# Kernel optimization log

Hardware: AMD Instinct MI355X
Metric: run time of the kernel (lower is better)

## Reference

```python
import jax, jax.numpy as jnp
import numpy as np

B, T, D_IN = 64, 512, 512      # batch, num_steps, input_size
S, HS, H = 8, 128, 8            # mem_slots, head_size, num_heads
M = HS * H                      # mem_size = 1024
KD = HS                         # key_size defaults to head_size
NG = 2 * M                      # num_gates (gate_style='unit')
N_MLP = 2                       # attention_mlp_layers (weights SHARED: [Linear]*2)
EPS = 1e-5


def _ln(x, g, b):
    mu = jnp.mean(x, axis=-1, keepdims=True)
    var = jnp.mean((x - mu) ** 2, axis=-1, keepdims=True)
    return (x - mu) * jax.lax.rsqrt(var + EPS) * g + b


def setup_inputs() -> dict:
    key = jax.random.key(0)
    ks = jax.random.split(key, 12)
    r = lambda i, shape, s=0.02: jax.random.normal(ks[i], shape, jnp.float32) * s
    return {
        "inputs": jax.random.normal(ks[0], (B, T, D_IN), jnp.float32),
        "memory": jax.random.normal(ks[1], (B, S, M), jnp.float32),
        "Wp": r(2, (D_IN, M)), "bp": jnp.zeros((M,), jnp.float32),
        "Wq": r(3, (M, KD * H)), "bq": jnp.zeros((KD * H,), jnp.float32),
        "Wk": r(4, (M, KD * H)), "bk": jnp.zeros((KD * H,), jnp.float32),
        "Wv": r(5, (M, HS * H)), "bv": jnp.zeros((HS * H,), jnp.float32),
        "Wm": r(6, (M, M)), "bm": jnp.zeros((M,), jnp.float32),
        "g1": jnp.ones((M,), jnp.float32), "be1": jnp.zeros((M,), jnp.float32),
        "g2": jnp.ones((M,), jnp.float32), "be2": jnp.zeros((M,), jnp.float32),
        "rl_w": r(7, (M,), 1.0),                       # RepeatLinear elementwise weight
        "rl_W": r(8, (M, NG)), "rl_b": jnp.zeros((NG,), jnp.float32),
        "gl_W": r(9, (S, M, NG)), "gl_b": r(10, (S, NG), 0.02),  # GroupLinearLayer
        "input_bias": jnp.float32(0.0),
        "forget_bias": jnp.float32(1.0),
    }


def reference(inputs, memory, Wp, bp, Wq, bq, Wk, bk, Wv, bv, Wm, bm,
              g1, be1, g2, be2, rl_w, rl_W, rl_b, gl_W, gl_b,
              input_bias, forget_bias):
    # forward_step with treat_input_as_matrix=True (single num_blocks=1 block)
    x = inputs @ Wp + bp                                   # [B,T,M] projected inputs
    # multihead attention: q from memory, k/v from inputs; NO 1/sqrt(d) scaling (as in source)
    q = (memory @ Wq + bq).reshape(B, S, H, KD).transpose(0, 2, 1, 3)   # [B,H,S,kd]
    k = (x @ Wk + bk).reshape(B, T, H, KD).transpose(0, 2, 1, 3)        # [B,H,T,kd]
    v = (x @ Wv + bv).reshape(B, T, H, HS).transpose(0, 2, 1, 3)        # [B,H,T,hs]
    scores = jax.nn.softmax(jnp.einsum('bhsd,bhtd->bhst', q, k), axis=-1)
    att = jnp.einsum('bhst,bhtd->bhsd', scores, v).transpose(0, 2, 1, 3).reshape(B, S, M)
    mem1 = _ln(memory + att, g1, be1)
    mlp = mem1
    for _ in range(N_MLP):  # ModuleList([Linear]*2) => same weights applied twice
        mlp = jax.nn.relu(mlp @ Wm + bm)
    next_memory = _ln(mem1 + mlp, g2, be2)
    # gates (create_gates uses ORIGINAL memory)
    gi = jnp.mean(jax.nn.relu(rl_w * x), axis=1) @ rl_W + rl_b            # [B,NG]
    gm = jnp.einsum('bsm,smg->bsg', jnp.tanh(memory), gl_W) + gl_b        # [B,S,NG]
    gates = gm + gi[:, None, :]
    ig = jax.nn.sigmoid(gates[..., :M] + input_bias)
    fg = jax.nn.sigmoid(gates[..., M:] + forget_bias)
    next_memory = ig * jnp.tanh(next_memory) + fg * memory
    return next_memory.reshape(B, S * M)
```

## Files before the change

kernel.cpp:

```cpp
#include <hip/hip_runtime.h>
#include <hip/hip_bf16.h>

#define Bq   64
#define Tt   512
#define DIN  512
#define Ss   8
#define HSs  128
#define Hh   8
#define Mm   1024
#define KDd  128
#define NGg  2048

typedef __attribute__((ext_vector_type(8))) short bf16x8;
typedef __attribute__((ext_vector_type(4))) float f32x4;

__device__ __forceinline__ ushort f2b(float f) {
    union { float f; unsigned u; } v; v.f = f;
    unsigned r = v.u + 0x7fffu + ((v.u >> 16) & 1u);
    return (ushort)(r >> 16);
}
__device__ __forceinline__ float b2f(ushort b) {
    union { unsigned u; float f; } v; v.u = ((unsigned)b) << 16;
    return v.f;
}
__device__ __forceinline__ float blo(unsigned u) {
    union { unsigned u; float f; } v; v.u = u << 16; return v.f;
}
__device__ __forceinline__ float bhi(unsigned u) {
    union { unsigned u; float f; } v; v.u = u & 0xffff0000u; return v.f;
}

#define GLOAD_LDS16(g, l) __builtin_amdgcn_global_load_lds( \
    (const __attribute__((address_space(1))) void*)(g),     \
    (__attribute__((address_space(3))) void*)(l), 16, 0, 0)

#define LGKM0 do { asm volatile("s_waitcnt lgkmcnt(0)" ::: "memory");         \
                   __builtin_amdgcn_sched_barrier(0); } while (0)

template<int OUT_BF16>
__global__ __launch_bounds__(512)
void gemm_big(const ushort* __restrict__ A, const ushort* __restrict__ Bt,
              const float* __restrict__ bias, void* __restrict__ Cout,
              int ldc, int Kdim)
{
    extern __shared__ __align__(16) char lds[];

    const int tid  = threadIdx.x;
    const int wid  = tid >> 6;
    const int lane = tid & 63;
    const int wy   = wid >> 2;
    const int wx   = wid & 3;

    const int gx   = gridDim.x;
    const int nwg  = gx * gridDim.y;
    const int orig = blockIdx.y * gx + blockIdx.x;
    const int q8   = nwg >> 3, r8 = nwg & 7;
    const int xcd  = orig & 7, idx8 = orig >> 3;
    const int swz  = (xcd < r8 ? xcd * (q8 + 1)
                               : r8 * (q8 + 1) + (xcd - r8) * q8) + idx8;
    const int row0 = (swz / gx) * 256;
    const int col0 = (swz % gx) * 256;

    const int NT = Kdim >> 6;

    const int sr = tid >> 3;
    const int sq = (tid & 7) ^ (sr & 7);
    const ushort* Asrc = A  + (size_t)(row0 + sr) * Kdim + sq * 8;
    const ushort* Bsrc = Bt + (size_t)(col0 + sr) * Kdim + sq * 8;
    const int ldsw = wid * 1024;

    auto stage = [&](int isB, int U, int h) {
        const ushort* s = (isB ? Bsrc : Asrc) + (size_t)h * 128 * Kdim
                        + (size_t)U * 64;
        char* d = lds + (isB ? 65536 : 0) + ((((U) & 1) * 2 + h) << 14) + ldsw;
        GLOAD_LDS16(s, d);
        GLOAD_LDS16(s + (size_t)64 * Kdim, d + 8192);
    };
    auto stage_tile = [&](int U) {
        stage(0, U, 0); stage(0, U, 1); stage(1, U, 0); stage(1, U, 1);
    };

    const int l15   = lane & 15;
    const int s0_16 = (((lane >> 4)) ^ (lane & 7)) << 4;
    const int s1_16 = ((4 + (lane >> 4)) ^ (lane & 7)) << 4;
    const int aoff  = wy * 8192 + l15 * 128;
    const int boff  = wx * 4096 + l15 * 128;

    f32x4 acc[4][4][2];
#pragma unroll
    for (int p = 0; p < 4; ++p)
#pragma unroll
        for (int m = 0; m < 4; ++m)
#pragma unroll
            for (int n = 0; n < 2; ++n) acc[p][m][n] = (f32x4){0.f,0.f,0.f,0.f};

#define MFMAQ(P, AH, BH)                                                      \
    {                                                                         \
        __builtin_amdgcn_s_setprio(1);                                        \
        _Pragma("unroll")                                                     \
        for (int kk = 0; kk < 2; ++kk)                                        \
            _Pragma("unroll")                                                 \
            for (int m = 0; m < 4; ++m)                                       \
                _Pragma("unroll")                                             \
                for (int n = 0; n < 2; ++n)                                   \
                    acc[P][m][n] = __builtin_amdgcn_mfma_f32_16x16x32_bf16(   \
                        AH[kk][m], BH[kk][n], acc[P][m][n], 0, 0, 0);         \
        __builtin_amdgcn_s_setprio(0);                                        \
    }

    stage_tile(0);
    stage_tile(1);
    asm volatile("s_waitcnt vmcnt(8)" ::: "memory");
    __builtin_amdgcn_s_barrier();
    asm volatile("" ::: "memory");

    for (int U = 0; U < NT; ++U) {
        const char* Ab = lds + ((U & 1) << 15);
        const char* Bb = lds + 65536 + ((U & 1) << 15);

        bf16x8 a0[2][4], a1[2][4];
        bf16x8 b0[2][2], b1[2][2];

#pragma unroll
        for (int m = 0; m < 4; ++m) {
            a0[0][m] = *(const bf16x8*)(Ab + aoff + s0_16 + m * 2048);
            a0[1][m] = *(const bf16x8*)(Ab + aoff + s1_16 + m * 2048);
        }
#pragma unroll
        for (int n = 0; n < 2; ++n) {
            b0[0][n] = *(const bf16x8*)(Bb + boff + s0_16 + n * 2048);
            b0[1][n] = *(const bf16x8*)(Bb + boff + s1_16 + n * 2048);
        }
        LGKM0;

#pragma unroll
        for (int m = 0; m < 4; ++m) {
            a1[0][m] = *(const bf16x8*)(Ab + 16384 + aoff + s0_16 + m * 2048);
            a1[1][m] = *(const bf16x8*)(Ab + 16384 + aoff + s1_16 + m * 2048);
        }
        MFMAQ(0, a0, b0);
        LGKM0;

#pragma unroll
        for (int n = 0; n < 2; ++n) {
            b1[0][n] = *(const bf16x8*)(Bb + 16384 + boff + s0_16 + n * 2048);
            b1[1][n] = *(const bf16x8*)(Bb + 16384 + boff + s1_16 + n * 2048);
        }
        MFMAQ(1, a1, b0);
        LGKM0;

        __builtin_amdgcn_s_barrier();
        asm volatile("" ::: "memory");
        if (U + 2 < NT) stage_tile(U + 2);

        MFMAQ(3, a1, b1);
        MFMAQ(2, a0, b1);

        if (U + 2 < NT) asm volatile("s_waitcnt vmcnt(8)" ::: "memory");
        else            asm volatile("s_waitcnt vmcnt(0)" ::: "memory");
        __builtin_amdgcn_s_barrier();
        asm volatile("" ::: "memory");
    }
#undef MFMAQ

#pragma unroll
    for (int p = 0; p < 4; ++p) {
        const int rb = row0 + (p & 1) * 128 + wy * 64 + (lane >> 4) * 4;
        const int cb = col0 + (p >> 1) * 128 + wx * 32 + (lane & 15);
#pragma unroll
        for (int n = 0; n < 2; ++n) {
            const float bv = bias[cb + n * 16];
#pragma unroll
            for (int m = 0; m < 4; ++m) {
#pragma unroll
                for (int r = 0; r < 4; ++r) {
                    const float v = acc[p][m][n][r] + bv;
                    const size_t off = (size_t)(rb + m * 16 + r) * ldc + cb + n * 16;
                    if (OUT_BF16) ((ushort*)Cout)[off] = f2b(v);
                    else          ((float*)Cout)[off]  = v;
                }
            }
        }
    }
}

template<int OUT_BF16, int RELU>
__global__ __launch_bounds__(256)
void gemm_sm(const ushort* __restrict__ A, const ushort* __restrict__ Bt,
             const float* __restrict__ bias, void* __restrict__ Cout,
             int ldc, int Kdim)
{
    __shared__ __align__(16) ushort As[128 * 32];
    __shared__ __align__(16) ushort Bs[128 * 32];

    const int tid  = threadIdx.x;
    const int w    = tid >> 6;
    const int lane = tid & 63;

    const int gx   = gridDim.x;
    const int nwg  = gx * gridDim.y;
    const int orig = blockIdx.y * gx + blockIdx.x;
    const int q8   = nwg >> 3, r8 = nwg & 7;
    const int xcd  = orig & 7, idx8 = orig >> 3;
    const int swz  = (xcd < r8 ? xcd * (q8 + 1)
                               : r8 * (q8 + 1) + (xcd - r8) * q8) + idx8;
    const int row0 = (swz / gx) * 128;
    const int col0 = (swz % gx) * 128;
    const int wr   = w >> 1, wc = w & 1;

    f32x4 acc[4][4];
#pragma unroll
    for (int i = 0; i < 4; ++i)
#pragma unroll
        for (int j = 0; j < 4; ++j) acc[i][j] = (f32x4){0.f, 0.f, 0.f, 0.f};

    const ushort* Ag = A  + (size_t)(row0 + (tid >> 2)) * Kdim + (tid & 3) * 8;
    const ushort* Bg = Bt + (size_t)(col0 + (tid >> 2)) * Kdim + (tid & 3) * 8;

    for (int k0 = 0; k0 < Kdim; k0 += 32) {
        __syncthreads();
#pragma unroll
        for (int is = 0; is < 2; ++is)
            GLOAD_LDS16(Ag + (size_t)is * 64 * Kdim + k0,
                        (char*)As + (is * 256 + w * 64) * 16);
#pragma unroll
        for (int is = 0; is < 2; ++is)
            GLOAD_LDS16(Bg + (size_t)is * 64 * Kdim + k0,
                        (char*)Bs + (is * 256 + w * 64) * 16);
        asm volatile("s_waitcnt vmcnt(0)" ::: "memory");
        __syncthreads();

        bf16x8 a[4], b[4];
#pragma unroll
        for (int i = 0; i < 4; ++i) {
            a[i] = *(const bf16x8*)&As[(wr * 64 + i * 16 + (lane & 15)) * 32 + (lane >> 4) * 8];
            b[i] = *(const bf16x8*)&Bs[(wc * 64 + i * 16 + (lane & 15)) * 32 + (lane >> 4) * 8];
        }
#pragma unroll
        for (int i = 0; i < 4; ++i)
#pragma unroll
            for (int j = 0; j < 4; ++j)
                acc[i][j] = __builtin_amdgcn_mfma_f32_16x16x32_bf16(a[i], b[j], acc[i][j], 0, 0, 0);
    }

    float bsv[4];
#pragma unroll
    for (int j = 0; j < 4; ++j) bsv[j] = bias[col0 + wc * 64 + j * 16 + (lane & 15)];
#pragma unroll
    for (int i = 0; i < 4; ++i) {
        const int row = row0 + wr * 64 + i * 16 + (lane >> 4) * 4;
        const int col = col0 + wc * 64 + (lane & 15);
#pragma unroll
        for (int r = 0; r < 4; ++r) {
            const size_t off = (size_t)(row + r) * ldc + col;
#pragma unroll
            for (int j = 0; j < 4; ++j) {
                float vv = acc[i][j][r] + bsv[j];
                if (RELU) vv = fmaxf(vv, 0.f);
                if (OUT_BF16) ((ushort*)Cout)[off + j * 16] = f2b(vv);
                else          ((float*)Cout)[off + j * 16]  = vv;
            }
        }
    }
}

__global__ __launch_bounds__(256)
void transpose_to_bf16(const float* __restrict__ in, ushort* __restrict__ out,
                       int R, int C)
{
    __shared__ float t[32][33];
    const int c0 = blockIdx.x * 32, r0 = blockIdx.y * 32;
    const int tx = threadIdx.x & 31, ty = threadIdx.x >> 5;
#pragma unroll
    for (int i = 0; i < 32; i += 8)
        t[ty + i][tx] = in[(size_t)(r0 + ty + i) * C + c0 + tx];
    __syncthreads();
#pragma unroll
    for (int i = 0; i < 32; i += 8)
        out[(size_t)(c0 + ty + i) * R + r0 + tx] = f2b(t[tx][ty + i]);
}

__global__ __launch_bounds__(256)
void conv_bf16(const float* __restrict__ in, ushort* __restrict__ out)
{
    const int i = blockIdx.x * 256 + threadIdx.x;
    float4 v = ((const float4*)in)[i];
    ushort4 o;
    o.x = f2b(v.x); o.y = f2b(v.y); o.z = f2b(v.z); o.w = f2b(v.w);
    ((ushort4*)out)[i] = o;
}

__global__ __launch_bounds__(256)
void fill0(float* __restrict__ o)
{
    o[blockIdx.x * 256 + threadIdx.x] = 0.f;
}

__global__ __launch_bounds__(256)
void fuse_bias(const float* __restrict__ bp,
               const float* __restrict__ Wk, const float* __restrict__ Wv,
               const float* __restrict__ bk, const float* __restrict__ bv,
               float* __restrict__ outb)
{
    __shared__ float red[4][64];
    const int col = threadIdx.x & 63;
    const int mq  = threadIdx.x >> 6;
    const int n   = blockIdx.x * 64 + col;
    const float* W = (n < Mm) ? Wk : Wv;
    const int nn   = n & (Mm - 1);
    float s = 0.f;
    for (int m = mq * 256; m < mq * 256 + 256; ++m)
        s += bp[m] * W[(size_t)m * Mm + nn];
    red[mq][col] = s;
    __syncthreads();
    if (mq == 0) {
        float t = red[0][col] + red[1][col] + red[2][col] + red[3][col];
        outb[n] = t + ((n < Mm) ? bk[nn] : bv[nn]);
    }
}

template<int BM, int BN, int BK, int TM, int TN, int SPLITK, bool TANH_A>
__global__ __launch_bounds__(256)
void gemm_f32_sk(const float* __restrict__ A, int lda, long long sA,
                 const float* __restrict__ B, int ldb, long long sB,
                 float* __restrict__ P, int Mrows, int Ncols, int Kdim)
{
    constexpr int TX = BN / TN;
    constexpr int TY = BM / TM;
    static_assert(TX * TY == 256, "256 threads");
    constexpr int KC4   = BK / 4;
    constexpr int A_PER = (BM * BK / 4) / 256;
    constexpr int B_PER = (BK * BN / 4) / 256;

    __shared__ float As[BK][BM + 4];
    __shared__ float Bs[BK][BN];

    const int tid = threadIdx.x;
    const int tx  = tid % TX;
    const int ty  = tid / TX;
    const int zz  = blockIdx.z;
    const int zb  = zz / SPLITK;
    const int ks  = zz % SPLITK;
    A += (long long)zb * sA;
    B += (long long)zb * sB;
    const int Kslice = Kdim / SPLITK;
    const int kbeg = ks * Kslice, kend = kbeg + Kslice;
    const int row0 = blockIdx.y * BM;
    const int col0 = blockIdx.x * BN;

    float acc[TM][TN];
#pragma unroll
    for (int i = 0; i < TM; ++i)
#pragma unroll
        for (int j = 0; j < TN; ++j) acc[i][j] = 0.f;

    for (int k0 = kbeg; k0 < kend; k0 += BK) {
        __syncthreads();
#pragma unroll
        for (int l = 0; l < A_PER; ++l) {
            int idx = tid + l * 256;
            int ar  = idx / KC4;
            int ac  = (idx % KC4) * 4;
            float4 va = *(const float4*)&A[(long long)(row0 + ar) * lda + k0 + ac];
            if (TANH_A) {
                va.x = tanhf(va.x); va.y = tanhf(va.y);
                va.z = tanhf(va.z); va.w = tanhf(va.w);
            }
            As[ac + 0][ar] = va.x;
            As[ac + 1][ar] = va.y;
            As[ac + 2][ar] = va.z;
            As[ac + 3][ar] = va.w;
        }
#pragma unroll
        for (int l = 0; l < B_PER; ++l) {
            int idx = tid + l * 256;
            int br  = idx / (BN / 4);
            int bc  = (idx % (BN / 4)) * 4;
            *(float4*)&Bs[br][bc] = *(const float4*)&B[(long long)(k0 + br) * ldb + col0 + bc];
        }
        __syncthreads();
#pragma unroll
        for (int k = 0; k < BK; ++k) {
            float a[TM], b[TN];
#pragma unroll
            for (int i = 0; i < TM; i += 4)
                *(float4*)&a[i] = *(const float4*)&As[k][ty * TM + i];
#pragma unroll
            for (int j = 0; j < TN; j += 4)
                *(float4*)&b[j] = *(const float4*)&Bs[k][tx * TN + j];
#pragma unroll
            for (int i = 0; i < TM; ++i)
#pragma unroll
                for (int j = 0; j < TN; ++j)
                    acc[i][j] = fmaf(a[i], b[j], acc[i][j]);
        }
    }

    float* Pz = P + (size_t)zz * Mrows * Ncols;
#pragma unroll
    for (int i = 0; i < TM; ++i) {
        const size_t prow = (size_t)(row0 + ty * TM + i) * Ncols;
#pragma unroll
        for (int j = 0; j < TN; j += 4)
            *(float4*)&Pz[prow + col0 + tx * TN + j] = *(const float4*)&acc[i][j];
    }
}

template<int SPLITK, bool RELU>
__global__ __launch_bounds__(256)
void sk_reduce(const float* __restrict__ P, const float* __restrict__ bias,
               long long sBias, float* __restrict__ C, int ldc, long long sC,
               int pb4, int Ncols)
{
    const int gid = blockIdx.x * 256 + threadIdx.x;
    const int batch = gid / pb4;
    const int r4    = gid % pb4;
    const float4* Pb = (const float4*)P + (size_t)batch * SPLITK * pb4 + r4;
    float4 s = Pb[0];
#pragma unroll
    for (int ks = 1; ks < SPLITK; ++ks) {
        float4 p = Pb[(size_t)ks * pb4];
        s.x += p.x; s.y += p.y; s.z += p.z; s.w += p.w;
    }
    const int col = (r4 * 4) % Ncols;
    const int row = (r4 * 4) / Ncols;
    float4 bv = *(const float4*)&bias[batch * sBias + col];
    s.x += bv.x; s.y += bv.y; s.z += bv.z; s.w += bv.w;
    if (RELU) {
        s.x = fmaxf(s.x, 0.f); s.y = fmaxf(s.y, 0.f);
        s.z = fmaxf(s.z, 0.f); s.w = fmaxf(s.w, 0.f);
    }
    *(float4*)&C[(size_t)batch * sC + (size_t)row * ldc + col] = s;
}

__global__ __launch_bounds__(256)
void gi_reduce(const ushort* __restrict__ x, const float* __restrict__ rl_w,
               float* __restrict__ gi_mean)
{
    const int b    = blockIdx.x / (Mm / 256);
    const int mblk = blockIdx.x % (Mm / 256);
    const int m    = mblk * 256 + threadIdx.x;
    const float w  = rl_w[m];
    const ushort* xp = x + (size_t)b * Tt * Mm + m;
    float sum = 0.f;
    for (int t = 0; t < Tt; ++t)
        sum += fmaxf(w * b2f(xp[(size_t)t * Mm]), 0.f);
    gi_mean[b * Mm + m] = sum * (1.f / (float)Tt);
}

__global__ __launch_bounds__(256)
void attn_kernel(const float* __restrict__ q, const ushort* __restrict__ kv,
                 float* __restrict__ att)
{
    const int b = blockIdx.x / Hh;
    const int h = blockIdx.x % Hh;
    const int tid = threadIdx.x;

    __shared__ float qs[Ss][KDd];
    __shared__ float sc[Ss][Tt];

    {
        int s  = tid / 32;
        int d4 = (tid % 32) * 4;
        float4 qv = *(const float4*)&q[((size_t)(b * Ss + s)) * Mm + h * KDd + d4];
        qs[s][d4 + 0] = qv.x; qs[s][d4 + 1] = qv.y;
        qs[s][d4 + 2] = qv.z; qs[s][d4 + 3] = qv.w;
    }
    __syncthreads();

#pragma unroll
    for (int half = 0; half < 2; ++half) {
        const int t = tid + half * 256;
        const ushort* kr = kv + ((size_t)(b * Tt + t)) * (2 * Mm) + h * KDd;
        float acc[Ss];
#pragma unroll
        for (int s = 0; s < Ss; ++s) acc[s] = 0.f;
        for (int d = 0; d < KDd; d += 8) {
            uint4 u = *(const uint4*)(kr + d);
            float k0 = blo(u.x), k1 = bhi(u.x), k2 = blo(u.y), k3 = bhi(u.y);
            float k4 = blo(u.z), k5 = bhi(u.z), k6 = blo(u.w), k7 = bhi(u.w);
#pragma unroll
            for (int s = 0; s < Ss; ++s)
                acc[s] += qs[s][d + 0] * k0 + qs[s][d + 1] * k1
                        + qs[s][d + 2] * k2 + qs[s][d + 3] * k3
                        + qs[s][d + 4] * k4 + qs[s][d + 5] * k5
                        + qs[s][d + 6] * k6 + qs[s][d + 7] * k7;
        }
#pragma unroll
        for (int s = 0; s < Ss; ++s) sc[s][t] = acc[s];
    }
    __syncthreads();

    const int s    = tid >> 5;
    const int lane = tid & 31;
    float mx = -1e30f;
    for (int t = lane; t < Tt; t += 32) mx = fmaxf(mx, sc[s][t]);
#pragma unroll
    for (int m = 16; m >= 1; m >>= 1) mx = fmaxf(mx, __shfl_xor(mx, m));
    float sum = 0.f;
    for (int t = lane; t < Tt; t += 32) {
        float e = __expf(sc[s][t] - mx);
        sc[s][t] = e;
        sum += e;
    }
#pragma unroll
    for (int m = 16; m >= 1; m >>= 1) sum += __shfl_xor(sum, m);
    const float inv = 1.f / sum;
    __syncthreads();

    const int d0 = (tid & 31) * 4;
    const ushort* vb = kv + ((size_t)(b * Tt)) * (2 * Mm) + Mm + h * KDd + d0;
    float4 acc = make_float4(0.f, 0.f, 0.f, 0.f);
    for (int t = 0; t < Tt; ++t) {
        const float p = sc[s][t];
        uint2 u = *(const uint2*)(vb + (size_t)t * (2 * Mm));
        acc.x = fmaf(p, blo(u.x), acc.x);
        acc.y = fmaf(p, bhi(u.x), acc.y);
        acc.z = fmaf(p, blo(u.y), acc.z);
        acc.w = fmaf(p, bhi(u.y), acc.w);
    }
    float4 o = make_float4(acc.x * inv, acc.y * inv, acc.z * inv, acc.w * inv);
    *(float4*)&att[((size_t)(b * Ss + s)) * Mm + h * KDd + d0] = o;
}

__global__ __launch_bounds__(256)
void ln_add(const float* __restrict__ a, const float* __restrict__ b,
            const float* __restrict__ g, const float* __restrict__ be,
            float* __restrict__ out)
{
    const int row = blockIdx.x;
    const int tid = threadIdx.x;
    const float* ap = a + (size_t)row * Mm;
    const float* bp = b + (size_t)row * Mm;

    float4 av = *(const float4*)&ap[tid * 4];
    float4 bv = *(const float4*)&bp[tid * 4];
    float x0 = av.x + bv.x, x1 = av.y + bv.y, x2 = av.z + bv.z, x3 = av.w + bv.w;
    float s  = x0 + x1 + x2 + x3;
    float ss = x0 * x0 + x1 * x1 + x2 * x2 + x3 * x3;
#pragma unroll
    for (int m = 32; m >= 1; m >>= 1) {
        s  += __shfl_xor(s, m);
        ss += __shfl_xor(ss, m);
    }
    __shared__ float red[2][4];
    const int wid = tid >> 6;
    if ((tid & 63) == 0) { red[0][wid] = s; red[1][wid] = ss; }
    __syncthreads();
    s  = red[0][0] + red[0][1] + red[0][2] + red[0][3];
    ss = red[1][0] + red[1][1] + red[1][2] + red[1][3];
    const float mu  = s * (1.f / (float)Mm);
    const float var = ss * (1.f / (float)Mm) - mu * mu;
    const float inv = rsqrtf(var + 1e-5f);

    float4 gv = *(const float4*)&g[tid * 4];
    float4 bev = *(const float4*)&be[tid * 4];
    float4 o;
    o.x = (x0 - mu) * inv * gv.x + bev.x;
    o.y = (x1 - mu) * inv * gv.y + bev.y;
    o.z = (x2 - mu) * inv * gv.z + bev.z;
    o.w = (x3 - mu) * inv * gv.w + bev.w;
    *(float4*)&out[(size_t)row * Mm + tid * 4] = o;
}

__global__ __launch_bounds__(256)
void combine_kernel(const float* __restrict__ gm, const float* __restrict__ gi,
                    const float* __restrict__ nextm, const float* __restrict__ memory,
                    const float* __restrict__ ibp, const float* __restrict__ fbp,
                    float* __restrict__ out)
{
    const int idx = blockIdx.x * 256 + threadIdx.x;
    const int m  = idx & (Mm - 1);
    const int bs = idx >> 10;
    const int b  = bs >> 3;
    const float ib = ibp[0], fb = fbp[0];
    const float gmi = gm[(size_t)bs * NGg + m];
    const float gmf = gm[(size_t)bs * NGg + Mm + m];
    const float gii = gi[(size_t)b * NGg + m];
    const float gif = gi[(size_t)b * NGg + Mm + m];
    const float ig = 1.f / (1.f + __expf(-(gmi + gii + ib)));
    const float fg = 1.f / (1.f + __expf(-(gmf + gif + fb)));
    out[idx] = ig * tanhf(nextm[idx]) + fg * memory[idx];
}

extern "C" void kernel_launch(void* const* d_in, const int* in_sizes, int n_in,
                              void* d_out, int out_size, void* d_ws, size_t ws_size,
                              hipStream_t stream)
{
    const float* inputs = (const float*)d_in[0];
    const float* memory = (const float*)d_in[1];
    const float* Wp  = (const float*)d_in[2];
    const float* bp  = (const float*)d_in[3];
    const float* Wq  = (const float*)d_in[4];
    const float* bq  = (const float*)d_in[5];
    const float* Wk  = (const float*)d_in[6];
    const float* bk  = (const float*)d_in[7];
    const float* Wv  = (const float*)d_in[8];
    const float* bv  = (const float*)d_in[9];
    const float* Wm  = (const float*)d_in[10];
    const float* bm  = (const float*)d_in[11];
    const float* g1  = (const float*)d_in[12];
    const float* be1 = (const float*)d_in[13];
    const float* g2  = (const float*)d_in[14];
    const float* be2 = (const float*)d_in[15];
    const float* rl_w = (const float*)d_in[16];
    const float* rl_W = (const float*)d_in[17];
    const float* rl_b = (const float*)d_in[18];
    const float* gl_W = (const float*)d_in[19];
    const float* gl_b = (const float*)d_in[20];
    const float* ibp  = (const float*)d_in[21];
    const float* fbp  = (const float*)d_in[22];
    float* out = (float*)d_out;

    (void)hipFuncSetAttribute(reinterpret_cast<const void*>(&gemm_big<1>),
                              hipFuncAttributeMaxDynamicSharedMemorySize, 131072);

    const size_t N_SM = (size_t)Bq * Ss * Mm;
    float* ws = (float*)d_ws;
    float* qbuf   = ws;
    float* attb   = qbuf   + N_SM;
    float* mem1   = attb   + N_SM;
    float* mlp1   = mem1   + N_SM;
    float* mlp2   = mlp1   + N_SM;
    float* nextm  = mlp2   + N_SM;
    float* tm     = nextm  + N_SM;
    float* gimean = tm     + N_SM;
    float* gibuf  = gimean + (size_t)Bq * Mm;
    float* gmbuf  = gibuf  + (size_t)Bq * NGg;
    float* skp    = gmbuf  + (size_t)Bq * Ss * NGg;
    const size_t SKP_FLOATS = (size_t)8 * 512 * 1024;
    float* bkvf   = skp + SKP_FLOATS;
    float* bz     = bkvf + NGg;
    float* pconst = bz + 512;
    ushort* ib16  = (ushort*)pconst;
    ushort* WpT   = ib16  + (size_t)Bq * Tt * DIN;
    ushort* WkvT  = WpT   + (size_t)Mm * DIN;
    ushort* WqT   = WkvT  + (size_t)2 * Mm * Mm;
    ushort* WmT   = WqT   + (size_t)Mm * Mm;
    ushort* mem16 = WmT   + (size_t)Mm * Mm;
    ushort* m116  = mem16 + N_SM;
    ushort* mlp116= m116  + N_SM;
    ushort* Wp16  = mlp116 + N_SM;
    ushort* WpkvT = Wp16  + (size_t)DIN * Mm;
    ushort* cend  = WpkvT + (size_t)2 * Mm * DIN;
    size_t const_u16 = (size_t)(cend - (ushort*)pconst);
    size_t const_floats = (size_t)(pconst - ws) + (const_u16 + 1) / 2;
    const_floats = (const_floats + 3) & ~(size_t)3;
    float* cstart = ws + const_floats;

    int Bc = Bq;
    while (Bc > 1 &&
           (const_floats + (size_t)Bc * Tt * Mm * 3 / 2) * sizeof(float) > ws_size)
        Bc >>= 1;
    const size_t N_XC = (size_t)Bc * Tt * Mm;
    ushort* kvb16 = (ushort*)cstart;
    ushort* xb16  = kvb16 + 2 * N_XC;

    const dim3 blk(256);

    conv_bf16<<<dim3((Bq * Tt * DIN) / 1024), blk, 0, stream>>>(inputs, ib16);
    conv_bf16<<<dim3((Bq * Ss * Mm) / 1024), blk, 0, stream>>>(memory, mem16);
    conv_bf16<<<dim3((DIN * Mm) / 1024), blk, 0, stream>>>(Wp, Wp16);
    transpose_to_bf16<<<dim3(Mm / 32, DIN / 32), blk, 0, stream>>>(Wp, WpT, DIN, Mm);
    transpose_to_bf16<<<dim3(Mm / 32, Mm / 32), blk, 0, stream>>>(Wk, WkvT, Mm, Mm);
    transpose_to_bf16<<<dim3(Mm / 32, Mm / 32), blk, 0, stream>>>(Wv, WkvT + (size_t)Mm * Mm, Mm, Mm);
    transpose_to_bf16<<<dim3(Mm / 32, Mm / 32), blk, 0, stream>>>(Wq, WqT, Mm, Mm);
    transpose_to_bf16<<<dim3(Mm / 32, Mm / 32), blk, 0, stream>>>(Wm, WmT, Mm, Mm);
    fill0<<<dim3(2), blk, 0, stream>>>(bz);

    gemm_sm<1,0><<<dim3(DIN/128, (2*Mm)/128), blk, 0, stream>>>(
        WkvT, Wp16, bz, WpkvT, DIN, Mm);

    fuse_bias<<<dim3(NGg / 64), blk, 0, stream>>>(bp, Wk, Wv, bk, bv, bkvf);

    gemm_sm<0,0><<<dim3(Mm/128, (Bq*Ss)/128), blk, 0, stream>>>(
        mem16, WqT, bq, qbuf, Mm, Mm);

    for (int c0 = 0; c0 < Bq; c0 += Bc) {
        const int rows = Bc * Tt;

        gemm_big<1><<<dim3((2*Mm)/256, rows/256), dim3(512), 131072, stream>>>(
            ib16 + (size_t)c0 * Tt * DIN, WpkvT, bkvf, kvb16, 2*Mm, DIN);

        gemm_big<1><<<dim3(Mm/256, rows/256), dim3(512), 131072, stream>>>(
            ib16 + (size_t)c0 * Tt * DIN, WpT, bp, xb16, Mm, DIN);

        gi_reduce<<<dim3(Bc * (Mm/256)), blk, 0, stream>>>(
            xb16, rl_w, gimean + (size_t)c0 * Mm);

        attn_kernel<<<dim3(Bc * Hh), blk, 0, stream>>>(
            qbuf + (size_t)c0 * Ss * Mm, kvb16,
            attb + (size_t)c0 * Ss * Mm);
    }

    ln_add<<<dim3(Bq * Ss), blk, 0, stream>>>(memory, attb, g1, be1, mem1);
    conv_bf16<<<dim3((Bq * Ss * Mm) / 1024), blk, 0, stream>>>(mem1, m116);

    gemm_sm<1,1><<<dim3(Mm/128, (Bq*Ss)/128), blk, 0, stream>>>(
        m116, WmT, bm, mlp116, Mm, Mm);
    gemm_sm<0,1><<<dim3(Mm/128, (Bq*Ss)/128), blk, 0, stream>>>(
        mlp116, WmT, bm, mlp2, Mm, Mm);

    ln_add<<<dim3(Bq * Ss), blk, 0, stream>>>(mem1, mlp2, g2, be2, nextm);

    gemm_f32_sk<64,64,16,4,4,4,true><<<dim3(NGg/64, Bq/64, Ss*4), blk, 0, stream>>>(
        memory, Ss*Mm, (long long)Mm,
        gl_W, NGg, (long long)Mm * NGg,
        skp, Bq, NGg, Mm);
    sk_reduce<4,false><<<dim3((Ss*Bq*NGg)/1024), blk, 0, stream>>>(
        skp, gl_b, NGg, gmbuf, Ss*NGg, NGg, (Bq*NGg)/4, NGg);

    gemm_f32_sk<64,64,16,4,4,8,false><<<dim3(NGg/64, Bq/64, 8), blk, 0, stream>>>(
        gimean, Mm, 0, rl_W, NGg, 0, skp, Bq, NGg, Mm);
    sk_reduce<8,false><<<dim3((Bq*NGg)/1024), blk, 0, stream>>>(
        skp, rl_b, 0, gibuf, NGg, 0, (Bq*NGg)/4, NGg);

    combine_kernel<<<dim3((Bq*Ss*Mm)/256), blk, 0, stream>>>(
        gmbuf, gibuf, nextm, memory, ibp, fbp, out);
}
```

Measured before the change: 492.5 us.

## Fuse x/K/V projection GEMMs and move group-linear gate GEMM to bf16 MFMA

```diff
diff --git a/kernel.cpp b/kernel.cpp
--- a/kernel.cpp
+++ b/kernel.cpp
@@ -10,6 +10,7 @@
 #define Mm   1024
 #define KDd  128
 #define NGg  2048
+#define KVS  3072
 
 typedef __attribute__((ext_vector_type(8))) short bf16x8;
 typedef __attribute__((ext_vector_type(4))) float f32x4;
@@ -265,6 +266,68 @@
 }
 
 __global__ __launch_bounds__(256)
+void gm_mfma(const ushort* __restrict__ tanhA, const ushort* __restrict__ glWT,
+             const float* __restrict__ gl_b, float* __restrict__ gm)
+{
+    __shared__ __align__(16) ushort As[64 * 32];
+    __shared__ __align__(16) ushort Bs[128 * 32];
+
+    const int tid  = threadIdx.x;
+    const int w    = tid >> 6;
+    const int lane = tid & 63;
+    const int s    = blockIdx.z;
+    const int col0 = blockIdx.x * 128;
+
+    f32x4 acc[4][2];
+#pragma unroll
+    for (int i = 0; i < 4; ++i)
+#pragma unroll
+        for (int j = 0; j < 2; ++j) acc[i][j] = (f32x4){0.f, 0.f, 0.f, 0.f};
+
+    const ushort* Ag = tanhA + (size_t)(tid >> 2) * (Ss * Mm) + s * Mm + (tid & 3) * 8;
+    const ushort* Bg = glWT + (size_t)s * NGg * Mm
+                     + (size_t)(col0 + (tid >> 2)) * Mm + (tid & 3) * 8;
+
+    for (int k0 = 0; k0 < Mm; k0 += 32) {
+        __syncthreads();
+        GLOAD_LDS16(Ag + k0, (char*)As + w * 1024);
+#pragma unroll
+        for (int is = 0; is < 2; ++is)
+            GLOAD_LDS16(Bg + (size_t)is * 64 * Mm + k0,
+                        (char*)Bs + (is * 256 + w * 64) * 16);
+        asm volatile("s_waitcnt vmcnt(0)" ::: "memory");
+        __syncthreads();
+
+        bf16x8 a[4], b[2];
+#pragma unroll
+        for (int i = 0; i < 4; ++i)
+            a[i] = *(const bf16x8*)&As[(i * 16 + (lane & 15)) * 32 + (lane >> 4) * 8];
+#pragma unroll
+        for (int j = 0; j < 2; ++j)
+            b[j] = *(const bf16x8*)&Bs[(w * 32 + j * 16 + (lane & 15)) * 32 + (lane >> 4) * 8];
+#pragma unroll
+        for (int i = 0; i < 4; ++i)
+#pragma unroll
+            for (int j = 0; j < 2; ++j)
+                acc[i][j] = __builtin_amdgcn_mfma_f32_16x16x32_bf16(a[i], b[j], acc[i][j], 0, 0, 0);
+    }
+
+#pragma unroll
+    for (int j = 0; j < 2; ++j) {
+        const int col = col0 + w * 32 + j * 16 + (lane & 15);
+        const float bv = gl_b[s * NGg + col];
+#pragma unroll
+        for (int i = 0; i < 4; ++i) {
+#pragma unroll
+            for (int r = 0; r < 4; ++r) {
+                const int b = i * 16 + (lane >> 4) * 4 + r;
+                gm[(size_t)b * (Ss * NGg) + (size_t)s * NGg + col] = acc[i][j][r] + bv;
+            }
+        }
+    }
+}
+
+__global__ __launch_bounds__(256)
 void transpose_to_bf16(const float* __restrict__ in, ushort* __restrict__ out,
                        int R, int C)
 {
@@ -291,9 +354,27 @@
 }
 
 __global__ __launch_bounds__(256)
+void tanh_bf16(const float* __restrict__ in, ushort* __restrict__ out)
+{
+    const int i = blockIdx.x * 256 + threadIdx.x;
+    float4 v = ((const float4*)in)[i];
+    ushort4 o;
+    o.x = f2b(tanhf(v.x)); o.y = f2b(tanhf(v.y));
+    o.z = f2b(tanhf(v.z)); o.w = f2b(tanhf(v.w));
+    ((ushort4*)out)[i] = o;
+}
+
+__global__ __launch_bounds__(256)
 void fill0(float* __restrict__ o)
 {
     o[blockIdx.x * 256 + threadIdx.x] = 0.f;
+}
+
+__global__ __launch_bounds__(256)
+void copy_vec(const float* __restrict__ in, float* __restrict__ o)
+{
+    const int i = blockIdx.x * 256 + threadIdx.x;
+    o[i] = in[i];
 }
 
 __global__ __launch_bounds__(256)
@@ -434,17 +515,17 @@
 }
 
 __global__ __launch_bounds__(256)
-void gi_reduce(const ushort* __restrict__ x, const float* __restrict__ rl_w,
+void gi_reduce(const ushort* __restrict__ kvx, const float* __restrict__ rl_w,
                float* __restrict__ gi_mean)
 {
     const int b    = blockIdx.x / (Mm / 256);
     const int mblk = blockIdx.x % (Mm / 256);
     const int m    = mblk * 256 + threadIdx.x;
     const float w  = rl_w[m];
-    const ushort* xp = x + (size_t)b * Tt * Mm + m;
+    const ushort* xp = kvx + (size_t)b * Tt * KVS + 2048 + m;
     float sum = 0.f;
     for (int t = 0; t < Tt; ++t)
-        sum += fmaxf(w * b2f(xp[(size_t)t * Mm]), 0.f);
+        sum += fmaxf(w * b2f(xp[(size_t)t * KVS]), 0.f);
     gi_mean[b * Mm + m] = sum * (1.f / (float)Tt);
 }
 
@@ -471,7 +552,7 @@
 #pragma unroll
     for (int half = 0; half < 2; ++half) {
         const int t = tid + half * 256;
-        const ushort* kr = kv + ((size_t)(b * Tt + t)) * (2 * Mm) + h * KDd;
+        const ushort* kr = kv + ((size_t)(b * Tt + t)) * KVS + h * KDd;
         float acc[Ss];
 #pragma unroll
         for (int s = 0; s < Ss; ++s) acc[s] = 0.f;
@@ -509,11 +590,11 @@
     __syncthreads();
 
     const int d0 = (tid & 31) * 4;
-    const ushort* vb = kv + ((size_t)(b * Tt)) * (2 * Mm) + Mm + h * KDd + d0;
+    const ushort* vb = kv + ((size_t)(b * Tt)) * KVS + Mm + h * KDd + d0;
     float4 acc = make_float4(0.f, 0.f, 0.f, 0.f);
     for (int t = 0; t < Tt; ++t) {
         const float p = sc[s][t];
-        uint2 u = *(const uint2*)(vb + (size_t)t * (2 * Mm));
+        uint2 u = *(const uint2*)(vb + (size_t)t * KVS);
         acc.x = fmaf(p, blo(u.x), acc.x);
         acc.y = fmaf(p, bhi(u.x), acc.y);
         acc.z = fmaf(p, blo(u.y), acc.z);
@@ -623,26 +704,26 @@
     float* mlp1   = mem1   + N_SM;
     float* mlp2   = mlp1   + N_SM;
     float* nextm  = mlp2   + N_SM;
-    float* tm     = nextm  + N_SM;
-    float* gimean = tm     + N_SM;
+    float* gimean = nextm  + N_SM;
     float* gibuf  = gimean + (size_t)Bq * Mm;
     float* gmbuf  = gibuf  + (size_t)Bq * NGg;
     float* skp    = gmbuf  + (size_t)Bq * Ss * NGg;
     const size_t SKP_FLOATS = (size_t)8 * 512 * 1024;
-    float* bkvf   = skp + SKP_FLOATS;
-    float* bz     = bkvf + NGg;
+    float* bkvx   = skp + SKP_FLOATS;
+    float* bz     = bkvx + KVS;
     float* pconst = bz + 512;
     ushort* ib16  = (ushort*)pconst;
-    ushort* WpT   = ib16  + (size_t)Bq * Tt * DIN;
-    ushort* WkvT  = WpT   + (size_t)Mm * DIN;
+    ushort* Wp16  = ib16  + (size_t)Bq * Tt * DIN;
+    ushort* WkvT  = Wp16  + (size_t)DIN * Mm;
     ushort* WqT   = WkvT  + (size_t)2 * Mm * Mm;
     ushort* WmT   = WqT   + (size_t)Mm * Mm;
     ushort* mem16 = WmT   + (size_t)Mm * Mm;
     ushort* m116  = mem16 + N_SM;
     ushort* mlp116= m116  + N_SM;
-    ushort* Wp16  = mlp116 + N_SM;
-    ushort* WpkvT = Wp16  + (size_t)DIN * Mm;
-    ushort* cend  = WpkvT + (size_t)2 * Mm * DIN;
+    ushort* kvxBt = mlp116 + N_SM;
+    ushort* glWT  = kvxBt + (size_t)KVS * DIN;
+    ushort* tanh16= glWT  + (size_t)Ss * NGg * Mm;
+    ushort* cend  = tanh16 + N_SM;
     size_t const_u16 = (size_t)(cend - (ushort*)pconst);
     size_t const_floats = (size_t)(pconst - ws) + (const_u16 + 1) / 2;
     const_floats = (const_floats + 3) & ~(size_t)3;
@@ -652,26 +733,30 @@
     while (Bc > 1 &&
            (const_floats + (size_t)Bc * Tt * Mm * 3 / 2) * sizeof(float) > ws_size)
         Bc >>= 1;
-    const size_t N_XC = (size_t)Bc * Tt * Mm;
-    ushort* kvb16 = (ushort*)cstart;
-    ushort* xb16  = kvb16 + 2 * N_XC;
+    ushort* kvxb16 = (ushort*)cstart;
 
     const dim3 blk(256);
 
     conv_bf16<<<dim3((Bq * Tt * DIN) / 1024), blk, 0, stream>>>(inputs, ib16);
     conv_bf16<<<dim3((Bq * Ss * Mm) / 1024), blk, 0, stream>>>(memory, mem16);
     conv_bf16<<<dim3((DIN * Mm) / 1024), blk, 0, stream>>>(Wp, Wp16);
-    transpose_to_bf16<<<dim3(Mm / 32, DIN / 32), blk, 0, stream>>>(Wp, WpT, DIN, Mm);
+    tanh_bf16<<<dim3((Bq * Ss * Mm) / 1024), blk, 0, stream>>>(memory, tanh16);
     transpose_to_bf16<<<dim3(Mm / 32, Mm / 32), blk, 0, stream>>>(Wk, WkvT, Mm, Mm);
     transpose_to_bf16<<<dim3(Mm / 32, Mm / 32), blk, 0, stream>>>(Wv, WkvT + (size_t)Mm * Mm, Mm, Mm);
     transpose_to_bf16<<<dim3(Mm / 32, Mm / 32), blk, 0, stream>>>(Wq, WqT, Mm, Mm);
     transpose_to_bf16<<<dim3(Mm / 32, Mm / 32), blk, 0, stream>>>(Wm, WmT, Mm, Mm);
+    transpose_to_bf16<<<dim3(Mm / 32, DIN / 32), blk, 0, stream>>>(
+        Wp, kvxBt + (size_t)NGg * DIN, DIN, Mm);
+    for (int s = 0; s < Ss; ++s)
+        transpose_to_bf16<<<dim3(NGg / 32, Mm / 32), blk, 0, stream>>>(
+            gl_W + (size_t)s * Mm * NGg, glWT + (size_t)s * NGg * Mm, Mm, NGg);
     fill0<<<dim3(2), blk, 0, stream>>>(bz);
 
     gemm_sm<1,0><<<dim3(DIN/128, (2*Mm)/128), blk, 0, stream>>>(
-        WkvT, Wp16, bz, WpkvT, DIN, Mm);
-
-    fuse_bias<<<dim3(NGg / 64), blk, 0, stream>>>(bp, Wk, Wv, bk, bv, bkvf);
+        WkvT, Wp16, bz, kvxBt, DIN, Mm);
+
+    fuse_bias<<<dim3(NGg / 64), blk, 0, stream>>>(bp, Wk, Wv, bk, bv, bkvx);
+    copy_vec<<<dim3(Mm / 256), blk, 0, stream>>>(bp, bkvx + NGg);
 
     gemm_sm<0,0><<<dim3(Mm/128, (Bq*Ss)/128), blk, 0, stream>>>(
         mem16, WqT, bq, qbuf, Mm, Mm);
@@ -679,17 +764,14 @@
     for (int c0 = 0; c0 < Bq; c0 += Bc) {
         const int rows = Bc * Tt;
 
-        gemm_big<1><<<dim3((2*Mm)/256, rows/256), dim3(512), 131072, stream>>>(
-            ib16 + (size_t)c0 * Tt * DIN, WpkvT, bkvf, kvb16, 2*Mm, DIN);
-
-        gemm_big<1><<<dim3(Mm/256, rows/256), dim3(512), 131072, stream>>>(
-            ib16 + (size_t)c0 * Tt * DIN, WpT, bp, xb16, Mm, DIN);
+        gemm_big<1><<<dim3(KVS/256, rows/256), dim3(512), 131072, stream>>>(
+            ib16 + (size_t)c0 * Tt * DIN, kvxBt, bkvx, kvxb16, KVS, DIN);
 
         gi_reduce<<<dim3(Bc * (Mm/256)), blk, 0, stream>>>(
-            xb16, rl_w, gimean + (size_t)c0 * Mm);
+            kvxb16, rl_w, gimean + (size_t)c0 * Mm);
 
         attn_kernel<<<dim3(Bc * Hh), blk, 0, stream>>>(
-            qbuf + (size_t)c0 * Ss * Mm, kvb16,
+            qbuf + (size_t)c0 * Ss * Mm, kvxb16,
             attb + (size_t)c0 * Ss * Mm);
     }
 
@@ -703,12 +785,7 @@
 
     ln_add<<<dim3(Bq * Ss), blk, 0, stream>>>(mem1, mlp2, g2, be2, nextm);
 
-    gemm_f32_sk<64,64,16,4,4,4,true><<<dim3(NGg/64, Bq/64, Ss*4), blk, 0, stream>>>(
-        memory, Ss*Mm, (long long)Mm,
-        gl_W, NGg, (long long)Mm * NGg,
-        skp, Bq, NGg, Mm);
-    sk_reduce<4,false><<<dim3((Ss*Bq*NGg)/1024), blk, 0, stream>>>(
-        skp, gl_b, NGg, gmbuf, Ss*NGg, NGg, (Bq*NGg)/4, NGg);
+    gm_mfma<<<dim3(NGg/128, 1, Ss), blk, 0, stream>>>(tanh16, glWT, gl_b, gmbuf);
 
     gemm_f32_sk<64,64,16,4,4,8,false><<<dim3(NGg/64, Bq/64, 8), blk, 0, stream>>>(
         gimean, Mm, 0, rl_W, NGg, 0, skp, Bq, NGg, Mm);
```

Result: slower. 510.9 us (+3.7%).

## Compute group-linear memory gates with bf16 MFMA directly, dropping split-K fp32 path

Applied to the files above, without the earlier changes.

```diff
diff --git a/kernel.cpp b/kernel.cpp
--- a/kernel.cpp
+++ b/kernel.cpp
@@ -265,6 +265,49 @@
 }
 
 __global__ __launch_bounds__(256)
+void gm_direct(const ushort* __restrict__ tanhA, const float* __restrict__ glW,
+               const float* __restrict__ gl_b, float* __restrict__ gm)
+{
+    const int tid  = threadIdx.x;
+    const int w    = tid >> 6;
+    const int lane = tid & 63;
+    const int s    = blockIdx.y;
+    const int n    = blockIdx.x * 64 + w * 16 + (lane & 15);
+    const int q8   = (lane >> 4) * 8;
+
+    const float* Bp = glW + (size_t)s * Mm * NGg + n;
+
+    f32x4 acc[4];
+#pragma unroll
+    for (int i = 0; i < 4; ++i) acc[i] = (f32x4){0.f, 0.f, 0.f, 0.f};
+
+#pragma unroll 2
+    for (int k0 = 0; k0 < Mm; k0 += 32) {
+        bf16x8 a[4];
+#pragma unroll
+        for (int i = 0; i < 4; ++i)
+            a[i] = *(const bf16x8*)&tanhA[((size_t)(i * 16 + (lane & 15)) * Ss + s) * Mm + k0 + q8];
+        bf16x8 bv;
+#pragma unroll
+        for (int j = 0; j < 8; ++j)
+            bv[j] = (short)f2b(Bp[(size_t)(k0 + q8 + j) * NGg]);
+#pragma unroll
+        for (int i = 0; i < 4; ++i)
+            acc[i] = __builtin_amdgcn_mfma_f32_16x16x32_bf16(a[i], bv, acc[i], 0, 0, 0);
+    }
+
+    const float bb = gl_b[s * NGg + n];
+#pragma unroll
+    for (int i = 0; i < 4; ++i) {
+#pragma unroll
+        for (int r = 0; r < 4; ++r) {
+            const int b = i * 16 + (lane >> 4) * 4 + r;
+            gm[((size_t)b * Ss + s) * NGg + n] = acc[i][r] + bb;
+        }
+    }
+}
+
+__global__ __launch_bounds__(256)
 void transpose_to_bf16(const float* __restrict__ in, ushort* __restrict__ out,
                        int R, int C)
 {
@@ -287,6 +330,17 @@
     float4 v = ((const float4*)in)[i];
     ushort4 o;
     o.x = f2b(v.x); o.y = f2b(v.y); o.z = f2b(v.z); o.w = f2b(v.w);
+    ((ushort4*)out)[i] = o;
+}
+
+__global__ __launch_bounds__(256)
+void tanh_bf16(const float* __restrict__ in, ushort* __restrict__ out)
+{
+    const int i = blockIdx.x * 256 + threadIdx.x;
+    float4 v = ((const float4*)in)[i];
+    ushort4 o;
+    o.x = f2b(tanhf(v.x)); o.y = f2b(tanhf(v.y));
+    o.z = f2b(tanhf(v.z)); o.w = f2b(tanhf(v.w));
     ((ushort4*)out)[i] = o;
 }
 
@@ -319,7 +373,7 @@
     }
 }
 
-template<int BM, int BN, int BK, int TM, int TN, int SPLITK, bool TANH_A>
+template<int BM, int BN, int BK, int TM, int TN, int SPLITK>
 __global__ __launch_bounds__(256)
 void gemm_f32_sk(const float* __restrict__ A, int lda, long long sA,
                  const float* __restrict__ B, int ldb, long long sB,
@@ -362,10 +416,6 @@
             int ar  = idx / KC4;
             int ac  = (idx % KC4) * 4;
             float4 va = *(const float4*)&A[(long long)(row0 + ar) * lda + k0 + ac];
-            if (TANH_A) {
-                va.x = tanhf(va.x); va.y = tanhf(va.y);
-                va.z = tanhf(va.z); va.w = tanhf(va.w);
-            }
             As[ac + 0][ar] = va.x;
             As[ac + 1][ar] = va.y;
             As[ac + 2][ar] = va.z;
@@ -623,8 +673,7 @@
     float* mlp1   = mem1   + N_SM;
     float* mlp2   = mlp1   + N_SM;
     float* nextm  = mlp2   + N_SM;
-    float* tm     = nextm  + N_SM;
-    float* gimean = tm     + N_SM;
+    float* gimean = nextm  + N_SM;
     float* gibuf  = gimean + (size_t)Bq * Mm;
     float* gmbuf  = gibuf  + (size_t)Bq * NGg;
     float* skp    = gmbuf  + (size_t)Bq * Ss * NGg;
@@ -642,7 +691,8 @@
     ushort* mlp116= m116  + N_SM;
     ushort* Wp16  = mlp116 + N_SM;
     ushort* WpkvT = Wp16  + (size_t)DIN * Mm;
-    ushort* cend  = WpkvT + (size_t)2 * Mm * DIN;
+    ushort* tanh16= WpkvT + (size_t)2 * Mm * DIN;
+    ushort* cend  = tanh16 + N_SM;
     size_t const_u16 = (size_t)(cend - (ushort*)pconst);
     size_t const_floats = (size_t)(pconst - ws) + (const_u16 + 1) / 2;
     const_floats = (const_floats + 3) & ~(size_t)3;
@@ -661,6 +711,7 @@
     conv_bf16<<<dim3((Bq * Tt * DIN) / 1024), blk, 0, stream>>>(inputs, ib16);
     conv_bf16<<<dim3((Bq * Ss * Mm) / 1024), blk, 0, stream>>>(memory, mem16);
     conv_bf16<<<dim3((DIN * Mm) / 1024), blk, 0, stream>>>(Wp, Wp16);
+    tanh_bf16<<<dim3((Bq * Ss * Mm) / 1024), blk, 0, stream>>>(memory, tanh16);
     transpose_to_bf16<<<dim3(Mm / 32, DIN / 32), blk, 0, stream>>>(Wp, WpT, DIN, Mm);
     transpose_to_bf16<<<dim3(Mm / 32, Mm / 32), blk, 0, stream>>>(Wk, WkvT, Mm, Mm);
     transpose_to_bf16<<<dim3(Mm / 32, Mm / 32), blk, 0, stream>>>(Wv, WkvT + (size_t)Mm * Mm, Mm, Mm);
@@ -703,14 +754,9 @@
 
     ln_add<<<dim3(Bq * Ss), blk, 0, stream>>>(mem1, mlp2, g2, be2, nextm);
 
-    gemm_f32_sk<64,64,16,4,4,4,true><<<dim3(NGg/64, Bq/64, Ss*4), blk, 0, stream>>>(
-        memory, Ss*Mm, (long long)Mm,
-        gl_W, NGg, (long long)Mm * NGg,
-        skp, Bq, NGg, Mm);
-    sk_reduce<4,false><<<dim3((Ss*Bq*NGg)/1024), blk, 0, stream>>>(
-        skp, gl_b, NGg, gmbuf, Ss*NGg, NGg, (Bq*NGg)/4, NGg);
-
-    gemm_f32_sk<64,64,16,4,4,8,false><<<dim3(NGg/64, Bq/64, 8), blk, 0, stream>>>(
+    gm_direct<<<dim3(NGg / 64, Ss), blk, 0, stream>>>(tanh16, gl_W, gl_b, gmbuf);
+
+    gemm_f32_sk<64,64,16,4,4,8><<<dim3(NGg/64, Bq/64, 8), blk, 0, stream>>>(
         gimean, Mm, 0, rl_W, NGg, 0, skp, Bq, NGg, Mm);
     sk_reduce<8,false><<<dim3((Bq*NGg)/1024), blk, 0, stream>>>(
         skp, rl_b, 0, gibuf, NGg, 0, (Bq*NGg)/4, NGg);
```

Measured after the change: 474.5 us. -3.7%, faster.
